# Kernel optimization log

Hardware: AMD Instinct MI355X
Metric: run time of the kernel (lower is better)

Reference implementation:

```python
import jax, jax.numpy as jnp
import numpy as np

DIM = 512
HEADS = 4
DIM_HEAD = 64          # dim // 8
INNER = HEADS * DIM_HEAD  # 256
M_LANDMARKS = 256      # dim // 2
PINV_ITERS = 6
KS = 33                # residual_conv_kernel
LN_EPS = 1e-5


def setup_inputs() -> dict:
    key = jax.random.key(0)
    ks = jax.random.split(key, 6)
    B, N = 8, 4096
    x = jax.random.normal(ks[0], (B, N, DIM), dtype=jnp.float32)
    ln_g = jnp.ones((DIM,), jnp.float32)
    ln_b = jnp.zeros((DIM,), jnp.float32)
    w_qkv = jax.random.normal(ks[1], (DIM, 3 * INNER), jnp.float32) * 0.02
    w_out = jax.random.normal(ks[2], (INNER, DIM), jnp.float32) * 0.02
    b_out = jnp.zeros((DIM,), jnp.float32)
    # depthwise Conv2d(heads, heads, (33,1), groups=heads, bias=False): OIHW = (4,1,33,1)
    w_res = jax.random.normal(ks[3], (HEADS, 1, KS, 1), jnp.float32) * 0.05
    return dict(x=x, ln_g=ln_g, ln_b=ln_b, w_qkv=w_qkv, w_out=w_out, b_out=b_out, w_res=w_res)


def moore_penrose_pinv(x, iters=PINV_ITERS):
    # x: [B, H, m, m]
    abs_x = jnp.abs(x)
    col = abs_x.sum(-1)
    row = abs_x.sum(-2)
    z = jnp.swapaxes(x, -1, -2) / (jnp.max(col) * jnp.max(row))
    I = jnp.eye(x.shape[-1], dtype=x.dtype)
    for _ in range(iters):
        xz = x @ z
        z = 0.25 * z @ (13. * I - xz @ (15. * I - xz @ (7. * I - xz)))
    return z


def reference(x, ln_g, ln_b, w_qkv, w_out, b_out, w_res):
    B, N, D = x.shape
    h, dh, m = HEADS, DIM_HEAD, M_LANDMARKS
    l = N // m  # landmark group size (N chosen divisible by m, so no padding)

    # pre-norm LayerNorm
    mu = x.mean(-1, keepdims=True)
    var = ((x - mu) ** 2).mean(-1, keepdims=True)
    xn = (x - mu) / jnp.sqrt(var + LN_EPS) * ln_g + ln_b

    qkv = xn @ w_qkv  # [B, N, 3*INNER]
    q, k, v = jnp.split(qkv, 3, axis=-1)
    to_heads = lambda t: t.reshape(B, N, h, dh).transpose(0, 2, 1, 3)  # [B,h,N,dh]
    q, k, v = to_heads(q), to_heads(k), to_heads(v)
    q = q * (dh ** -0.5)

    # landmarks: mean over contiguous groups of l  ('b h (n l) d -> b h n d')
    q_l = q.reshape(B, h, m, l, dh).mean(3)  # [B,h,m,dh]
    k_l = k.reshape(B, h, m, l, dh).mean(3)

    sim1 = jnp.einsum('bhid,bhjd->bhij', q, k_l)    # [B,h,N,m]
    sim2 = jnp.einsum('bhid,bhjd->bhij', q_l, k_l)  # [B,h,m,m]
    sim3 = jnp.einsum('bhid,bhjd->bhij', q_l, k)    # [B,h,m,N]

    a1 = jax.nn.softmax(sim1, axis=-1)
    a2 = jax.nn.softmax(sim2, axis=-1)
    a3 = jax.nn.softmax(sim3, axis=-1)

    a2_inv = moore_penrose_pinv(a2)
    out = (a1 @ a2_inv) @ (a3 @ v)  # [B,h,N,dh]

    # residual depthwise conv on v along sequence: treat as NCHW with C=h, H=N, W=dh
    conv = jax.lax.conv_general_dilated(
        v, w_res, window_strides=(1, 1),
        padding=((KS // 2, KS // 2), (0, 0)),
        feature_group_count=h,
        dimension_numbers=('NCHW', 'OIHW', 'NCHW'))
    out = out + conv

    out = out.transpose(0, 2, 1, 3).reshape(B, N, h * dh)
    out = out @ w_out + b_out  # to_out (dropout=0.1 inactive in eval)
    return x + out
```

## Files before the change

kernel.cpp:

```cpp
#include <hip/hip_runtime.h>
#include <hip/hip_bf16.h>
#include <string.h>

typedef __hip_bfloat16 bf16;
typedef __attribute__((ext_vector_type(8))) __bf16 bf16x8;
typedef __attribute__((ext_vector_type(4))) float f32x4;
typedef __attribute__((ext_vector_type(8))) unsigned short u16x8;

#define NN 4096
#define DD 512
#define MM 256
#define ROWS 32768

__device__ __forceinline__ float b2f(bf16 x) { return __bfloat162float(x); }
__device__ __forceinline__ float u2f(unsigned short u) {
  return __uint_as_float(((unsigned int)u) << 16);
}
__device__ __forceinline__ unsigned short f2bu(float v) {
  bf16 h = __float2bfloat16(v);
  return *reinterpret_cast<unsigned short*>(&h);
}
__device__ __forceinline__ float ldf(const void* p, size_t i, int f) {
  return f ? ((const float*)p)[i] : __bfloat162float(((const bf16*)p)[i]);
}
__device__ __forceinline__ void stf(void* p, size_t i, float v, int f) {
  if (f) ((float*)p)[i] = v;
  else ((bf16*)p)[i] = __float2bfloat16(v);
}

__global__ void detect_kernel(const void* x, int* flag) {
  __shared__ int red[256];
  int tid = threadIdx.x;
  const unsigned short* u = (const unsigned short*)x;
  int local = 0;
  for (int i = 0; i < 32; i++) {
    unsigned short e = (u[tid * 32 + i] >> 7) & 0xFF;
    if (e >= 0xC8) local++;
  }
  red[tid] = local; __syncthreads();
  #pragma unroll
  for (int s = 128; s > 0; s >>= 1) {
    if (tid < s) red[tid] += red[tid + s];
    __syncthreads();
  }
  if (tid == 0) *flag = (red[0] > 32) ? 1 : 0;
}

__device__ __forceinline__ float bred_max(float v, float* red) {
  int tid = threadIdx.x;
  red[tid] = v; __syncthreads();
  #pragma unroll
  for (int s = 128; s > 0; s >>= 1) {
    if (tid < s) red[tid] = fmaxf(red[tid], red[tid + s]);
    __syncthreads();
  }
  float r = red[0]; __syncthreads();
  return r;
}
__device__ __forceinline__ float bred_sum(float v, float* red) {
  int tid = threadIdx.x;
  red[tid] = v; __syncthreads();
  #pragma unroll
  for (int s = 128; s > 0; s >>= 1) {
    if (tid < s) red[tid] += red[tid + s];
    __syncthreads();
  }
  float r = red[0]; __syncthreads();
  return r;
}

__global__ void ln_stats_kernel(const void* __restrict__ x, float* __restrict__ stats,
                                const int* dflag) {
  int f = *dflag;
  int wave = threadIdx.x >> 6, lane = threadIdx.x & 63;
  int row = blockIdx.x * 4 + wave;
  size_t base = (size_t)row * DD + lane * 8;
  float v[8];
  if (f) {
    const float* xp = (const float*)x + base;
    float4 a = *(const float4*)xp;
    float4 b = *(const float4*)(xp + 4);
    v[0] = a.x; v[1] = a.y; v[2] = a.z; v[3] = a.w;
    v[4] = b.x; v[5] = b.y; v[6] = b.z; v[7] = b.w;
  } else {
    const bf16* xp = (const bf16*)x + base;
    u16x8 t = *(const u16x8*)xp;
    #pragma unroll
    for (int e = 0; e < 8; e++) v[e] = u2f(t[e]);
  }
  float s = 0, s2 = 0;
  #pragma unroll
  for (int e = 0; e < 8; e++) { s += v[e]; s2 += v[e] * v[e]; }
  #pragma unroll
  for (int off = 1; off < 64; off <<= 1) {
    s += __shfl_xor(s, off);
    s2 += __shfl_xor(s2, off);
  }
  if (lane == 0) {
    float mean = s * (1.0f / DD);
    float var = s2 * (1.0f / DD) - mean * mean;
    stats[row * 2] = mean;
    stats[row * 2 + 1] = rsqrtf(var + 1e-5f);
  }
}

__global__ void transpose_kernel(const void* __restrict__ in, bf16* __restrict__ out,
                                 int R, int Cc, long sIn, long sOut,
                                 const int* dflag, int ovr) {
  int f = (ovr >= 0) ? ovr : *dflag;
  size_t o = (size_t)blockIdx.x * 256 + threadIdx.x;
  size_t per = (size_t)R * Cc;
  size_t b = o / per, rem = o % per;
  size_t c = rem / R, r = rem % R;
  out[b * sOut + c * (size_t)R + r] = __float2bfloat16(ldf(in, b * sIn + r * (size_t)Cc + c, f));
}

__global__ __launch_bounds__(256) void gemm_qkv(
    const void* __restrict__ x, const float* __restrict__ stats,
    const void* __restrict__ g, const void* __restrict__ bb,
    const bf16* __restrict__ wT,
    bf16* __restrict__ q, bf16* __restrict__ k, bf16* __restrict__ v,
    const int* __restrict__ dflag) {
  __shared__ __align__(16) unsigned short As[128][40];
  __shared__ __align__(16) unsigned short Bs[128][40];
  __shared__ __align__(16) float gls[512];
  __shared__ __align__(16) float bls[512];
  int f = *dflag;
  int tid = threadIdx.x;
  {
    int c0 = tid, c1 = tid + 256;
    gls[c0] = ldf(g, c0, f);  gls[c1] = ldf(g, c1, f);
    bls[c0] = ldf(bb, c0, f); bls[c1] = ldf(bb, c1, f);
  }
  int m0 = blockIdx.x * 128, n0 = blockIdx.y * 128;
  int sr = tid >> 1, sh = (tid & 1) * 16;
  int wave = tid >> 6, lane = tid & 63;
  int wm = (wave & 1) * 64, wn = (wave >> 1) * 64;
  int l15 = lane & 15, quad = lane >> 4;
  int r = m0 + sr;
  float mu = stats[r * 2], rs = stats[r * 2 + 1];
  const float* xf = (const float*)x + (size_t)r * DD;
  const bf16*  xb = (const bf16*)x  + (size_t)r * DD;
  __syncthreads();
  f32x4 acc[4][4] = {};
  for (int k0 = 0; k0 < 512; k0 += 32) {
    {
      float xv[16];
      if (f) {
        const float* src = xf + k0 + sh;
        float4 t0 = *(const float4*)(src);
        float4 t1 = *(const float4*)(src + 4);
        float4 t2 = *(const float4*)(src + 8);
        float4 t3 = *(const float4*)(src + 12);
        xv[0] = t0.x; xv[1] = t0.y; xv[2]  = t0.z; xv[3]  = t0.w;
        xv[4] = t1.x; xv[5] = t1.y; xv[6]  = t1.z; xv[7]  = t1.w;
        xv[8] = t2.x; xv[9] = t2.y; xv[10] = t2.z; xv[11] = t2.w;
        xv[12] = t3.x; xv[13] = t3.y; xv[14] = t3.z; xv[15] = t3.w;
      } else {
        const bf16* src = xb + k0 + sh;
        u16x8 t0 = *(const u16x8*)(src);
        u16x8 t1 = *(const u16x8*)(src + 8);
        #pragma unroll
        for (int e = 0; e < 8; e++) { xv[e] = u2f(t0[e]); xv[8 + e] = u2f(t1[e]); }
      }
      float gv[16], bv[16];
      {
        const float* gp = &gls[k0 + sh];
        const float* bp = &bls[k0 + sh];
        #pragma unroll
        for (int e4 = 0; e4 < 4; e4++) {
          float4 gt = *(const float4*)(gp + e4 * 4);
          float4 bt = *(const float4*)(bp + e4 * 4);
          gv[e4 * 4 + 0] = gt.x; gv[e4 * 4 + 1] = gt.y; gv[e4 * 4 + 2] = gt.z; gv[e4 * 4 + 3] = gt.w;
          bv[e4 * 4 + 0] = bt.x; bv[e4 * 4 + 1] = bt.y; bv[e4 * 4 + 2] = bt.z; bv[e4 * 4 + 3] = bt.w;
        }
      }
      u16x8 w0, w1;
      #pragma unroll
      for (int e = 0; e < 8; e++) {
        float a0 = rs * gv[e];
        float a1 = rs * gv[e + 8];
        w0[e] = f2bu(xv[e] * a0 + (bv[e] - mu * a0));
        w1[e] = f2bu(xv[e + 8] * a1 + (bv[e + 8] - mu * a1));
      }
      *(u16x8*)&As[sr][sh] = w0;
      *(u16x8*)&As[sr][sh + 8] = w1;
    }
    {
      const bf16* src = wT + (size_t)(n0 + sr) * 512 + k0 + sh;
      *(u16x8*)&Bs[sr][sh] = *(const u16x8*)src;
      *(u16x8*)&Bs[sr][sh + 8] = *(const u16x8*)(src + 8);
    }
    __syncthreads();
    bf16x8 af[4], bfr[4];
    #pragma unroll
    for (int i = 0; i < 4; i++) af[i] = *(const bf16x8*)&As[wm + i * 16 + l15][quad * 8];
    #pragma unroll
    for (int j = 0; j < 4; j++) bfr[j] = *(const bf16x8*)&Bs[wn + j * 16 + l15][quad * 8];
    #pragma unroll
    for (int i = 0; i < 4; i++)
      #pragma unroll
      for (int j = 0; j < 4; j++)
        acc[i][j] = __builtin_amdgcn_mfma_f32_16x16x32_bf16(af[i], bfr[j], acc[i][j], 0, 0, 0);
    __syncthreads();
  }
  float* eps = (float*)&As[0][0];
  int half = wave & 1;
  int er = tid >> 4, ec8 = (tid & 15) * 8;
  for (int p = 0; p < 8; p++) {
    if (half == (p >> 2)) {
      int i = p & 3;
      #pragma unroll
      for (int j = 0; j < 4; j++)
        #pragma unroll
        for (int reg = 0; reg < 4; reg++)
          eps[(quad * 4 + reg) * 132 + wn + j * 16 + l15] = acc[i][j][reg];
    }
    __syncthreads();
    {
      int row = m0 + p * 16 + er;
      int c = n0 + ec8;
      int which = c >> 8, h = (c >> 6) & 3, d = c & 63;
      int b_ = row >> 12, n = row & 4095;
      const float* src = &eps[er * 132 + ec8];
      float scale = (which == 0) ? 0.125f : 1.0f;
      u16x8 o;
      #pragma unroll
      for (int e = 0; e < 8; e++) o[e] = f2bu(src[e] * scale);
      bf16* dst = (which == 0) ? q : (which == 1) ? k : v;
      *(u16x8*)(dst + ((size_t)(b_ * 4 + h) * NN + n) * 64 + d) = o;
    }
    __syncthreads();
  }
}

__global__ __launch_bounds__(256) void gemm_bt(
    const bf16* __restrict__ A, long ldA, long sA,
    const bf16* __restrict__ Bt, long ldB, long sB,
    void* __restrict__ C, long ldC, long sC,
    int N, int kLen, int nTiles, int mode,
    const void* __restrict__ bias, const void* __restrict__ resid,
    const int* __restrict__ dflag) {
  __shared__ __align__(16) unsigned short As[128][40];
  __shared__ __align__(16) unsigned short Bs[128][40];
  int tid = threadIdx.x;
  int b = blockIdx.x;
  int m0 = blockIdx.y * 128;
  int nt = blockIdx.z % nTiles, ks = blockIdx.z / nTiles;
  int n0 = nt * 128;
  long k0b = (long)ks * kLen;
  const bf16* Ab = A + (size_t)b * sA;
  const bf16* Bb = Bt + (size_t)b * sB;
  int sr = tid >> 1, sh = (tid & 1) * 16;
  int wave = tid >> 6, lane = tid & 63;
  int wm = (wave & 1) * 64, wn = (wave >> 1) * 64;
  int l15 = lane & 15, quad = lane >> 4;
  f32x4 acc[4][4] = {};
  for (int kc = 0; kc < kLen; kc += 32) {
    long k0 = k0b + kc;
    {
      const bf16* src = Ab + (size_t)(m0 + sr) * ldA + k0 + sh;
      *(u16x8*)&As[sr][sh] = *(const u16x8*)src;
      *(u16x8*)&As[sr][sh + 8] = *(const u16x8*)(src + 8);
    }
    if (n0 + sr < N) {
      const bf16* src = Bb + (size_t)(n0 + sr) * ldB + k0 + sh;
      *(u16x8*)&Bs[sr][sh] = *(const u16x8*)src;
      *(u16x8*)&Bs[sr][sh + 8] = *(const u16x8*)(src + 8);
    } else {
      u16x8 z = {};
      *(u16x8*)&Bs[sr][sh] = z;
      *(u16x8*)&Bs[sr][sh + 8] = z;
    }
    __syncthreads();
    bf16x8 af[4], bfr[4];
    #pragma unroll
    for (int i = 0; i < 4; i++) af[i] = *(const bf16x8*)&As[wm + i * 16 + l15][quad * 8];
    #pragma unroll
    for (int j = 0; j < 4; j++) bfr[j] = *(const bf16x8*)&Bs[wn + j * 16 + l15][quad * 8];
    #pragma unroll
    for (int i = 0; i < 4; i++)
      #pragma unroll
      for (int j = 0; j < 4; j++)
        acc[i][j] = __builtin_amdgcn_mfma_f32_16x16x32_bf16(af[i], bfr[j], acc[i][j], 0, 0, 0);
    __syncthreads();
  }
  if (mode == 3) {
    int f = *dflag;
    float* eps = (float*)&As[0][0];
    int half = wave & 1;
    int er = tid >> 4, ec8 = (tid & 15) * 8;
    int colb = n0 + ec8;
    float bias8[8];
    #pragma unroll
    for (int e = 0; e < 8; e++) bias8[e] = ldf(bias, colb + e, f);
    for (int p = 0; p < 8; p++) {
      if (half == (p >> 2)) {
        int i = p & 3;
        #pragma unroll
        for (int j = 0; j < 4; j++)
          #pragma unroll
          for (int reg = 0; reg < 4; reg++)
            eps[(quad * 4 + reg) * 132 + wn + j * 16 + l15] = acc[i][j][reg];
      }
      __syncthreads();
      {
        int row = m0 + p * 16 + er;
        size_t off = (size_t)row * ldC + colb;
        const float* src = &eps[er * 132 + ec8];
        if (f) {
          float* Cp = (float*)C + off;
          const float* xr = (const float*)resid + off;
          float4 r0 = *(const float4*)xr;
          float4 r1 = *(const float4*)(xr + 4);
          float4 o0, o1;
          o0.x = src[0] + bias8[0] + r0.x; o0.y = src[1] + bias8[1] + r0.y;
          o0.z = src[2] + bias8[2] + r0.z; o0.w = src[3] + bias8[3] + r0.w;
          o1.x = src[4] + bias8[4] + r1.x; o1.y = src[5] + bias8[5] + r1.y;
          o1.z = src[6] + bias8[6] + r1.z; o1.w = src[7] + bias8[7] + r1.w;
          *(float4*)Cp = o0;
          *(float4*)(Cp + 4) = o1;
        } else {
          bf16* Cp = (bf16*)C + off;
          const bf16* xr = (const bf16*)resid + off;
          u16x8 rv = *(const u16x8*)xr;
          u16x8 o;
          #pragma unroll
          for (int e = 0; e < 8; e++) o[e] = f2bu(src[e] + bias8[e] + u2f(rv[e]));
          *(u16x8*)Cp = o;
        }
      }
      __syncthreads();
    }
    return;
  }
  #pragma unroll
  for (int i = 0; i < 4; i++)
    #pragma unroll
    for (int j = 0; j < 4; j++)
      #pragma unroll
      for (int reg = 0; reg < 4; reg++) {
        int row = m0 + wm + i * 16 + quad * 4 + reg;
        int col = n0 + wn + j * 16 + l15;
        if (col < N) {
          float val = acc[i][j][reg];
          size_t off = (size_t)row * ldC + col;
          if (mode == 0) (((float*)C) + (size_t)b * sC)[off] = val;
          else if (mode == 1) (((bf16*)C) + (size_t)b * sC)[off] = __float2bfloat16(val);
          else atomicAdd(((float*)C) + (size_t)b * sC + off, val);
        }
      }
}

__global__ void landmark_kernel(const bf16* __restrict__ src, float* __restrict__ dstf,
                                bf16* __restrict__ dstb) {
  int idx = blockIdx.x * 256 + threadIdx.x;
  int d = idx & 63, j = (idx >> 6) & 255, bh = idx >> 14;
  const bf16* s = src + ((size_t)bh * NN + j * 16) * 64 + d;
  float a = 0;
  #pragma unroll
  for (int i = 0; i < 16; i++) a += b2f(s[i * 64]);
  a *= (1.0f / 16);
  dstf[idx] = a;
  dstb[idx] = __float2bfloat16(a);
}

__global__ void a2_kernel(const float* __restrict__ ql, const float* __restrict__ kl,
                          float* __restrict__ a2) {
  __shared__ float qs[64];
  __shared__ float red[256];
  int bh = blockIdx.x >> 8, i = blockIdx.x & 255, tid = threadIdx.x;
  if (tid < 64) qs[tid] = ql[((size_t)bh * MM + i) * 64 + tid];
  __syncthreads();
  const float* kr = kl + ((size_t)bh * MM + tid) * 64;
  float s = 0;
  #pragma unroll
  for (int d = 0; d < 64; d++) s += qs[d] * kr[d];
  float mx = bred_max(s, red);
  float e = __expf(s - mx);
  float sm = bred_sum(e, red);
  a2[((size_t)bh * MM + i) * MM + tid] = e / sm;
}

__global__ void colsum_max_kernel(const float* __restrict__ a2, float* __restrict__ gmax) {
  __shared__ float red[256];
  int bh = blockIdx.x, tid = threadIdx.x;
  const float* base = a2 + (size_t)bh * MM * MM + tid;
  float s0 = 0, s1 = 0, s2 = 0, s3 = 0, s4 = 0, s5 = 0, s6 = 0, s7 = 0;
  for (int i = 0; i < 256; i += 8) {
    s0 += base[(size_t)(i + 0) * MM];
    s1 += base[(size_t)(i + 1) * MM];
    s2 += base[(size_t)(i + 2) * MM];
    s3 += base[(size_t)(i + 3) * MM];
    s4 += base[(size_t)(i + 4) * MM];
    s5 += base[(size_t)(i + 5) * MM];
    s6 += base[(size_t)(i + 6) * MM];
    s7 += base[(size_t)(i + 7) * MM];
  }
  float tot = ((s0 + s1) + (s2 + s3)) + ((s4 + s5) + (s6 + s7));
  float mx = bred_max(tot, red);
  if (tid == 0) atomicMax((int*)gmax + 1, __float_as_int(mx));
}

__global__ void zinit_kernel(const float* __restrict__ a2, const float* __restrict__ gmax,
                             float* __restrict__ z) {
  int idx = blockIdx.x * 256 + threadIdx.x;
  int j = idx & 255, i = (idx >> 8) & 255, bh = idx >> 16;
  float scale = 1.0f / gmax[1];
  z[idx] = a2[((size_t)bh * MM + j) * MM + i] * scale;
}

__global__ __launch_bounds__(256) void bmm64_mfma(
    const float* __restrict__ A, const float* __restrict__ B_,
    float* __restrict__ C,
    int Nn, int Kk, long sA, long sB, long sC,
    float alpha, float beta, float gbA, float gbB) {
  __shared__ __align__(16) unsigned short Ah[64][40];
  __shared__ __align__(16) unsigned short Al[64][40];
  __shared__ __align__(16) unsigned short Bh[64][40];
  __shared__ __align__(16) unsigned short Bl[64][40];
  int bh = blockIdx.x;
  int row0 = blockIdx.y * 64, col0 = blockIdx.z * 64;
  const float* Ab = A + (size_t)bh * sA;
  const float* Bb = B_ + (size_t)bh * sB;
  int tid = threadIdx.x;
  int wave = tid >> 6, lane = tid & 63, l15 = lane & 15, quad = lane >> 4;
  int wm = (wave & 1) * 32, wn = (wave >> 1) * 32;
  int ar2 = tid >> 2, kq = (tid & 3) * 8;
  int kr = tid >> 3, n8 = (tid & 7) * 8;
  f32x4 acc[2][2] = {};
  for (int k0 = 0; k0 < Kk; k0 += 32) {
    {
      const float* src = Ab + (size_t)(row0 + ar2) * Kk + k0 + kq;
      u16x8 hi, lo;
      #pragma unroll
      for (int e = 0; e < 8; e++) {
        float a = src[e];
        unsigned short h = f2bu(a);
        hi[e] = h;
        lo[e] = f2bu(a - u2f(h));
      }
      *(u16x8*)&Ah[ar2][kq] = hi;
      *(u16x8*)&Al[ar2][kq] = lo;
    }
    {
      const float* src = Bb + (size_t)(k0 + kr) * Nn + col0 + n8;
      int kk = k0 + kr;
      #pragma unroll
      for (int e = 0; e < 8; e++) {
        float b = gbB * src[e];
        if (kk == col0 + n8 + e) b += gbA;
        unsigned short h = f2bu(b);
        Bh[n8 + e][kr] = h;
        Bl[n8 + e][kr] = f2bu(b - u2f(h));
      }
    }
    __syncthreads();
    bf16x8 ah[2], al[2], bhf[2], blf[2];
    #pragma unroll
    for (int i = 0; i < 2; i++) {
      ah[i]  = *(const bf16x8*)&Ah[wm + i * 16 + l15][quad * 8];
      al[i]  = *(const bf16x8*)&Al[wm + i * 16 + l15][quad * 8];
      bhf[i] = *(const bf16x8*)&Bh[wn + i * 16 + l15][quad * 8];
      blf[i] = *(const bf16x8*)&Bl[wn + i * 16 + l15][quad * 8];
    }
    #pragma unroll
    for (int i = 0; i < 2; i++)
      #pragma unroll
      for (int j = 0; j < 2; j++) {
        acc[i][j] = __builtin_amdgcn_mfma_f32_16x16x32_bf16(ah[i], bhf[j], acc[i][j], 0, 0, 0);
        acc[i][j] = __builtin_amdgcn_mfma_f32_16x16x32_bf16(ah[i], blf[j], acc[i][j], 0, 0, 0);
        acc[i][j] = __builtin_amdgcn_mfma_f32_16x16x32_bf16(al[i], bhf[j], acc[i][j], 0, 0, 0);
      }
    __syncthreads();
  }
  #pragma unroll
  for (int i = 0; i < 2; i++)
    #pragma unroll
    for (int j = 0; j < 2; j++)
      #pragma unroll
      for (int reg = 0; reg < 4; reg++) {
        int r = row0 + wm + i * 16 + quad * 4 + reg;
        int cc = col0 + wn + j * 16 + l15;
        C[(size_t)bh * sC + (size_t)r * Nn + cc] = alpha * (r == cc) + beta * acc[i][j][reg];
      }
}

__global__ void wmsplit_kernel(const float* __restrict__ Wm, bf16* __restrict__ h,
                               bf16* __restrict__ l) {
  int o = blockIdx.x * 256 + threadIdx.x;
  int c = o & 255, d = (o >> 8) & 63, bh = o >> 14;
  float w = Wm[(((size_t)bh << 8) + c) * 64 + d];
  unsigned short hh = f2bu(w);
  h[o] = __float2bfloat16(w);
  l[o] = __float2bfloat16(w - u2f(hh));
}

__global__ __launch_bounds__(512) void sim3_flash_kernel(
    const bf16* __restrict__ qlbf, const bf16* __restrict__ k,
    const bf16* __restrict__ vT, float* __restrict__ a3v) {
  __shared__ __align__(16) unsigned short Qs[32][72];
  __shared__ __align__(16) unsigned short Pl[8][32][72];
  __shared__ __align__(16) float OW[32][64];
  __shared__ float mW[8][32];
  __shared__ float lW[8][32];
  int tid = threadIdx.x;
  int lt = blockIdx.x;
  int bh = blockIdx.y;
  int lm0 = lt * 32;
  if (tid < 256) {
    int r = tid >> 3, s = (tid & 7) * 8;
    *(u16x8*)&Qs[r][s] = *(const u16x8*)(qlbf + ((size_t)bh * 256 + lm0 + r) * 64 + s);
  }
  {
    float4 z = {};
    ((float4*)OW)[tid] = z;
  }
  __syncthreads();
  int wid = tid >> 6, lane = tid & 63, l15 = lane & 15, quad = lane >> 4;
  const bf16* kb = k + (size_t)bh * (NN * 64);
  const bf16* vb = vT + (size_t)bh * 262144;
  unsigned short* Pw = &Pl[wid][0][0];
  float m_[2] = {-1e30f, -1e30f};
  float l_[2] = {0.f, 0.f};
  f32x4 acc_o[2][4] = {};
  for (int ch = 0; ch < 8; ch++) {
    int kvb = wid * 512 + ch * 64;
    f32x4 acc_s[4][2] = {};
    #pragma unroll
    for (int kc = 0; kc < 2; kc++) {
      bf16x8 kf[4], qf[2];
      #pragma unroll
      for (int i = 0; i < 4; i++)
        kf[i] = *(const bf16x8*)(kb + (size_t)(kvb + i * 16 + l15) * 64 + kc * 32 + quad * 8);
      #pragma unroll
      for (int j = 0; j < 2; j++)
        qf[j] = *(const bf16x8*)&Qs[j * 16 + l15][kc * 32 + quad * 8];
      #pragma unroll
      for (int i = 0; i < 4; i++)
        #pragma unroll
        for (int j = 0; j < 2; j++)
          acc_s[i][j] = __builtin_amdgcn_mfma_f32_16x16x32_bf16(kf[i], qf[j], acc_s[i][j], 0, 0, 0);
    }
    float scl[2];
    #pragma unroll
    for (int js = 0; js < 2; js++) {
      float cm = acc_s[0][js][0];
      #pragma unroll
      for (int i = 0; i < 4; i++)
        #pragma unroll
        for (int reg = 0; reg < 4; reg++) cm = fmaxf(cm, acc_s[i][js][reg]);
      cm = fmaxf(cm, __shfl_xor(cm, 16));
      cm = fmaxf(cm, __shfl_xor(cm, 32));
      float mn = fmaxf(m_[js], cm);
      scl[js] = __expf(m_[js] - mn);
      m_[js] = mn;
    }
    #pragma unroll
    for (int io = 0; io < 2; io++)
      #pragma unroll
      for (int reg = 0; reg < 4; reg++) {
        float sb = __shfl(scl[io], quad * 4 + reg);
        #pragma unroll
        for (int jd = 0; jd < 4; jd++) acc_o[io][jd][reg] *= sb;
      }
    #pragma unroll
    for (int js = 0; js < 2; js++) {
      float cs = 0;
      #pragma unroll
      for (int i = 0; i < 4; i++)
        #pragma unroll
        for (int reg = 0; reg < 4; reg++) {
          float p = __expf(acc_s[i][js][reg] - m_[js]);
          cs += p;
          Pw[(js * 16 + l15) * 72 + i * 16 + quad * 4 + reg] = f2bu(p);
        }
      cs += __shfl_xor(cs, 16);
      cs += __shfl_xor(cs, 32);
      l_[js] = l_[js] * scl[js] + cs;
    }
    #pragma unroll
    for (int kc2 = 0; kc2 < 2; kc2++) {
      bf16x8 pf[2], vf[4];
      #pragma unroll
      for (int io = 0; io < 2; io++)
        pf[io] = *(const bf16x8*)&Pw[(io * 16 + l15) * 72 + kc2 * 32 + quad * 8];
      #pragma unroll
      for (int jd = 0; jd < 4; jd++)
        vf[jd] = *(const bf16x8*)(vb + (size_t)(jd * 16 + l15) * 4096 + kvb + kc2 * 32 + quad * 8);
      #pragma unroll
      for (int io = 0; io < 2; io++)
        #pragma unroll
        for (int jd = 0; jd < 4; jd++)
          acc_o[io][jd] = __builtin_amdgcn_mfma_f32_16x16x32_bf16(pf[io], vf[jd], acc_o[io][jd], 0, 0, 0);
    }
  }
  if (quad == 0) {
    mW[wid][l15] = m_[0]; mW[wid][16 + l15] = m_[1];
    lW[wid][l15] = l_[0]; lW[wid][16 + l15] = l_[1];
  }
  __syncthreads();
  #pragma unroll
  for (int io = 0; io < 2; io++)
    #pragma unroll
    for (int reg = 0; reg < 4; reg++) {
      int lm = io * 16 + quad * 4 + reg;
      float ms = mW[0][lm];
      #pragma unroll
      for (int w = 1; w < 8; w++) ms = fmaxf(ms, mW[w][lm]);
      float ls = 0;
      #pragma unroll
      for (int w = 0; w < 8; w++) ls += __expf(mW[w][lm] - ms) * lW[w][lm];
      float fac = __expf(mW[wid][lm] - ms) / ls;
      #pragma unroll
      for (int jd = 0; jd < 4; jd++)
        atomicAdd(&OW[lm][jd * 16 + l15], acc_o[io][jd][reg] * fac);
    }
  __syncthreads();
  {
    float4 o = ((float4*)OW)[tid];
    *(float4*)(a3v + (size_t)bh * 16384 + (size_t)lm0 * 64 + tid * 4) = o;
  }
}

__global__ __launch_bounds__(256) void attn1_pv_kernel(
    const bf16* __restrict__ q, const bf16* __restrict__ klbf,
    const bf16* __restrict__ wmt_h, const bf16* __restrict__ wmt_l,
    float* __restrict__ p1f, int bh0) {
  __shared__ __align__(16) unsigned short Qs[32][72];
  __shared__ __align__(16) unsigned short Ks[256][72];
  __shared__ __align__(16) unsigned short Wh[64][40];
  __shared__ __align__(16) unsigned short Wl[64][40];
  __shared__ float redm[4][32];
  __shared__ float reds[4][32];
  int tid = threadIdx.x;
  int bhl = blockIdx.y, bh = bh0 + bhl;
  int n0 = blockIdx.x * 32;
  const bf16* qb = q + ((size_t)bh * NN + n0) * 64;
  const bf16* kb = klbf + (size_t)bh * 16384;
  {
    int r = tid >> 3, s = (tid & 7) * 8;
    *(u16x8*)&Qs[r][s] = *(const u16x8*)(qb + (size_t)r * 64 + s);
  }
  {
    const bf16* src = kb + (size_t)tid * 64;
    #pragma unroll
    for (int s8 = 0; s8 < 8; s8++) *(u16x8*)&Ks[tid][s8 * 8] = *(const u16x8*)(src + s8 * 8);
  }
  __syncthreads();
  int wave = tid >> 6, lane = tid & 63, l15 = lane & 15, quad = lane >> 4;
  f32x4 acc[2][4] = {};
  #pragma unroll
  for (int kc = 0; kc < 64; kc += 32) {
    bf16x8 af[2], bfr[4];
    #pragma unroll
    for (int i = 0; i < 2; i++) af[i] = *(const bf16x8*)&Qs[i * 16 + l15][kc + quad * 8];
    #pragma unroll
    for (int j = 0; j < 4; j++) bfr[j] = *(const bf16x8*)&Ks[wave * 64 + j * 16 + l15][kc + quad * 8];
    #pragma unroll
    for (int i = 0; i < 2; i++)
      #pragma unroll
      for (int j = 0; j < 4; j++)
        acc[i][j] = __builtin_amdgcn_mfma_f32_16x16x32_bf16(af[i], bfr[j], acc[i][j], 0, 0, 0);
  }
  float lm[2][4], ls[2][4], rinv[2][4];
  #pragma unroll
  for (int i = 0; i < 2; i++)
    #pragma unroll
    for (int reg = 0; reg < 4; reg++)
      lm[i][reg] = fmaxf(fmaxf(acc[i][0][reg], acc[i][1][reg]),
                         fmaxf(acc[i][2][reg], acc[i][3][reg]));
  #pragma unroll
  for (int off = 1; off < 16; off <<= 1)
    #pragma unroll
    for (int i = 0; i < 2; i++)
      #pragma unroll
      for (int reg = 0; reg < 4; reg++) lm[i][reg] = fmaxf(lm[i][reg], __shfl_xor(lm[i][reg], off));
  if (l15 == 0)
    #pragma unroll
    for (int i = 0; i < 2; i++)
      #pragma unroll
      for (int reg = 0; reg < 4; reg++) redm[wave][i * 16 + quad * 4 + reg] = lm[i][reg];
  __syncthreads();
  #pragma unroll
  for (int i = 0; i < 2; i++)
    #pragma unroll
    for (int reg = 0; reg < 4; reg++) {
      int r = i * 16 + quad * 4 + reg;
      rinv[i][reg] = fmaxf(fmaxf(redm[0][r], redm[1][r]), fmaxf(redm[2][r], redm[3][r]));
      ls[i][reg] = 0;
    }
  #pragma unroll
  for (int i = 0; i < 2; i++)
    #pragma unroll
    for (int j = 0; j < 4; j++)
      #pragma unroll
      for (int reg = 0; reg < 4; reg++) {
        float e = __expf(acc[i][j][reg] - rinv[i][reg]);
        acc[i][j][reg] = e;
        ls[i][reg] += e;
      }
  #pragma unroll
  for (int off = 1; off < 16; off <<= 1)
    #pragma unroll
    for (int i = 0; i < 2; i++)
      #pragma unroll
      for (int reg = 0; reg < 4; reg++) ls[i][reg] += __shfl_xor(ls[i][reg], off);
  if (l15 == 0)
    #pragma unroll
    for (int i = 0; i < 2; i++)
      #pragma unroll
      for (int reg = 0; reg < 4; reg++) reds[wave][i * 16 + quad * 4 + reg] = ls[i][reg];
  __syncthreads();
  #pragma unroll
  for (int i = 0; i < 2; i++)
    #pragma unroll
    for (int reg = 0; reg < 4; reg++) {
      int r = i * 16 + quad * 4 + reg;
      rinv[i][reg] = 1.0f / (reds[0][r] + reds[1][r] + reds[2][r] + reds[3][r]);
    }
  unsigned short* Pb = &Ks[0][0];
  #pragma unroll
  for (int i = 0; i < 2; i++)
    #pragma unroll
    for (int j = 0; j < 4; j++)
      #pragma unroll
      for (int reg = 0; reg < 4; reg++) {
        float pv = acc[i][j][reg] * rinv[i][reg];
        unsigned short h = f2bu(pv);
        int row = i * 16 + quad * 4 + reg;
        int col = wave * 64 + j * 16 + l15;
        Pb[row * 264 + col] = h;
        Pb[8448 + row * 264 + col] = f2bu(pv - u2f(h));
      }
  const bf16* whp = wmt_h + (size_t)bh * 16384;
  const bf16* wlp = wmt_l + (size_t)bh * 16384;
  int wd = tid >> 2, wc = (tid & 3) * 8;
  int iw = wave & 1, dw = (wave >> 1) * 32;
  f32x4 accp[2] = {};
  for (int kc = 0; kc < 256; kc += 32) {
    __syncthreads();
    *(u16x8*)&Wh[wd][wc] = *(const u16x8*)(whp + (size_t)wd * 256 + kc + wc);
    *(u16x8*)&Wl[wd][wc] = *(const u16x8*)(wlp + (size_t)wd * 256 + kc + wc);
    __syncthreads();
    bf16x8 ah = *(const bf16x8*)&Pb[(iw * 16 + l15) * 264 + kc + quad * 8];
    bf16x8 al = *(const bf16x8*)&Pb[8448 + (iw * 16 + l15) * 264 + kc + quad * 8];
    #pragma unroll
    for (int jj = 0; jj < 2; jj++) {
      bf16x8 bh2 = *(const bf16x8*)&Wh[dw + jj * 16 + l15][quad * 8];
      bf16x8 bl2 = *(const bf16x8*)&Wl[dw + jj * 16 + l15][quad * 8];
      accp[jj] = __builtin_amdgcn_mfma_f32_16x16x32_bf16(ah, bh2, accp[jj], 0, 0, 0);
      accp[jj] = __builtin_amdgcn_mfma_f32_16x16x32_bf16(ah, bl2, accp[jj], 0, 0, 0);
      accp[jj] = __builtin_amdgcn_mfma_f32_16x16x32_bf16(al, bh2, accp[jj], 0, 0, 0);
    }
  }
  #pragma unroll
  for (int jj = 0; jj < 2; jj++)
    #pragma unroll
    for (int reg = 0; reg < 4; reg++) {
      int r = iw * 16 + quad * 4 + reg;
      int d = dw + jj * 16 + l15;
      int n = n0 + r;
      p1f[((size_t)bhl * NN + n) * 64 + d] = accp[jj][reg];
    }
}

__global__ __launch_bounds__(256) void conv_add_kernel(
    const float* __restrict__ p1, const bf16* __restrict__ v,
    const void* __restrict__ wres, bf16* __restrict__ y, const int* __restrict__ dflag,
    int bh0) {
  __shared__ __align__(16) unsigned short Vs[96][64];
  int f = *dflag;
  int tid = threadIdx.x;
  int bhl = blockIdx.y, bh = bh0 + bhl;
  int n0 = blockIdx.x * 64;
  int h = bh & 3, b_ = bh >> 2;
  const bf16* vb = v + (size_t)bh * (NN * 64);
  for (int rr = tid; rr < 384; rr += 256) {
    int r = rr >> 2, s = (rr & 3) * 16;
    int n = n0 - 16 + r;
    if (n >= 0 && n < NN) {
      *(u16x8*)&Vs[r][s] = *(const u16x8*)(vb + (size_t)n * 64 + s);
      *(u16x8*)&Vs[r][s + 8] = *(const u16x8*)(vb + (size_t)n * 64 + s + 8);
    } else {
      u16x8 z = {};
      *(u16x8*)&Vs[r][s] = z; *(u16x8*)&Vs[r][s + 8] = z;
    }
  }
  float w33[33];
  #pragma unroll
  for (int kk = 0; kk < 33; kk++) w33[kk] = ldf(wres, h * 33 + kk, f);
  __syncthreads();
  int d = tid & 63, rb = tid >> 6;
  for (int ii = 0; ii < 16; ii++) {
    int nl = ii * 4 + rb;
    float cv = 0;
    #pragma unroll
    for (int kk = 0; kk < 33; kk++) cv += w33[kk] * u2f(Vs[nl + kk][d]);
    int n = n0 + nl;
    float pv = p1[((size_t)bhl * NN + n) * 64 + d];
    y[((size_t)b_ * NN + n) * 256 + h * 64 + d] = __float2bfloat16(pv + cv);
  }
}

extern "C" void kernel_launch(void* const* d_in, const int* in_sizes, int n_in,
                              void* d_out, int out_size, void* d_ws, size_t ws_size,
                              hipStream_t stream) {
  const void* x     = d_in[0];
  const void* ln_g  = d_in[1];
  const void* ln_b  = d_in[2];
  const void* w_qkv = d_in[3];
  const void* w_out = d_in[4];
  const void* b_out = d_in[5];
  const void* w_res = d_in[6];

  float* ws    = (float*)d_ws;
  float* gmax  = ws;
  int*   dflag = (int*)(ws + 2);
  float* stats = ws + 256;
  bf16*  woutT = (bf16*)(stats + 65536);
  float* qlf   = (float*)(stats + 65536 + 65536);
  float* klf   = qlf + 524288;
  bf16*  qlbf  = (bf16*)(klf + 524288);
  bf16*  klbf  = qlbf + 524288;
  float* a3v   = (float*)(klbf + 524288);
  float* Wm    = a3v + 524288;
  float* a2    = Wm + 524288;
  bf16*  q     = (bf16*)(a2 + 2097152);
  bf16*  k     = q + 8388608;
  bf16*  v     = k + 8388608;
  bf16*  y     = k;
  bf16*  wmt_h = (bf16*)a2;
  bf16*  wmt_l = wmt_h + 524288;

  char* dob = (char*)d_out;
  bf16* wqkvT = (bf16*)dob;
  bf16* vTfull = (bf16*)dob;
  float* W0   = (float*)dob;
  float* W1   = (float*)(dob + (8u << 20));
  float* W2   = (float*)(dob + (16u << 20));
  float* W3   = (float*)(dob + (24u << 20));
  float* p1f  = (float*)dob;

  detect_kernel<<<1, 256, 0, stream>>>(x, dflag);
  hipMemsetAsync(gmax, 0, 2 * sizeof(float), stream);
  ln_stats_kernel<<<8192, 256, 0, stream>>>(x, stats, dflag);

  transpose_kernel<<<1536, 256, 0, stream>>>(w_qkv, wqkvT, 512, 768, 0, 0, dflag, -1);
  transpose_kernel<<<512, 256, 0, stream>>>(w_out, woutT, 256, 512, 0, 0, dflag, -1);

  gemm_qkv<<<dim3(256, 6), 256, 0, stream>>>(x, stats, ln_g, ln_b, wqkvT, q, k, v, dflag);

  landmark_kernel<<<2048, 256, 0, stream>>>(q, qlf, qlbf);
  landmark_kernel<<<2048, 256, 0, stream>>>(k, klf, klbf);

  transpose_kernel<<<32768, 256, 0, stream>>>(v, vTfull, 4096, 64, 262144, 262144, dflag, 0);
  sim3_flash_kernel<<<dim3(8, 32), 512, 0, stream>>>(qlbf, k, vTfull, a3v);

  a2_kernel<<<8192, 256, 0, stream>>>(qlf, klf, a2);
  colsum_max_kernel<<<32, 256, 0, stream>>>(a2, gmax);
  zinit_kernel<<<8192, 256, 0, stream>>>(a2, gmax, W0);

  float* zi = W0; float* f1 = W1; float* f2 = W2; float* f3 = W3;
  for (int it = 0; it < 6; it++) {
    bmm64_mfma<<<dim3(32, 4, 4), 256, 0, stream>>>(a2, zi, f1, 256, 256, 65536, 65536, 65536, 0.f, 1.f, 0.f, 1.f);
    bmm64_mfma<<<dim3(32, 4, 4), 256, 0, stream>>>(f1, f1, f2, 256, 256, 65536, 65536, 65536, 15.f, -1.f, 7.f, -1.f);
    bmm64_mfma<<<dim3(32, 4, 4), 256, 0, stream>>>(f1, f2, f3, 256, 256, 65536, 65536, 65536, 13.f, -1.f, 0.f, 1.f);
    bmm64_mfma<<<dim3(32, 4, 4), 256, 0, stream>>>(zi, f3, f2, 256, 256, 65536, 65536, 65536, 0.f, 0.25f, 0.f, 1.f);
    float* nzi = f2; f2 = f1; f1 = zi; zi = nzi;
  }

  bmm64_mfma<<<dim3(32, 4, 1), 256, 0, stream>>>(zi, a3v, Wm, 64, 256, 65536, 16384, 16384, 0.f, 1.f, 0.f, 1.f);

  wmsplit_kernel<<<2048, 256, 0, stream>>>(Wm, wmt_h, wmt_l);

  attn1_pv_kernel<<<dim3(128, 32), 256, 0, stream>>>(q, klbf, wmt_h, wmt_l, p1f, 0);
  conv_add_kernel<<<dim3(64, 32), 256, 0, stream>>>(p1f, v, w_res, y, dflag, 0);

  gemm_bt<<<dim3(1, 256, 4), 256, 0, stream>>>(
      y, 256, 0, woutT, 256, 0,
      d_out, 512, 0, 512, 256, 4, 3, b_out, x, dflag);
}
```

Measured before the change: 850.1 us.

## Fuse residual depthwise conv into attn1 PV kernel and drop LDS staging of Wm

Merges the separate conv_add kernel into the attn1 PV kernel, so the fp32 intermediate p1f (32x4096x64 floats) is never written to and re-read from global memory, and one launch is removed. The Wm hi/lo operands are now loaded straight from global memory (cached) instead of being staged through shared memory with two barriers per k-chunk. P hi/lo bf16 stores are packed into 32-bit LDS writes using lane shuffles. The conv reuses the Ks shared buffer for a 64-row V halo tile. This adds conv work and V loads to each block, and the direct global B-operand loads may have more latency.

```diff
diff --git a/kernel.cpp b/kernel.cpp
--- a/kernel.cpp
+++ b/kernel.cpp
@@ -623,19 +623,21 @@
   }
 }
 
-__global__ __launch_bounds__(256) void attn1_pv_kernel(
+__global__ __launch_bounds__(256) void attn1_pv_conv_kernel(
     const bf16* __restrict__ q, const bf16* __restrict__ klbf,
     const bf16* __restrict__ wmt_h, const bf16* __restrict__ wmt_l,
-    float* __restrict__ p1f, int bh0) {
+    const bf16* __restrict__ v, const void* __restrict__ wres,
+    bf16* __restrict__ y, const int* __restrict__ dflag) {
   __shared__ __align__(16) unsigned short Qs[32][72];
   __shared__ __align__(16) unsigned short Ks[256][72];
-  __shared__ __align__(16) unsigned short Wh[64][40];
-  __shared__ __align__(16) unsigned short Wl[64][40];
   __shared__ float redm[4][32];
   __shared__ float reds[4][32];
+  __shared__ float wls[33];
   int tid = threadIdx.x;
-  int bhl = blockIdx.y, bh = bh0 + bhl;
+  int bh = blockIdx.y;
   int n0 = blockIdx.x * 32;
+  int h = bh & 3, b_ = bh >> 2;
+  if (tid < 33) wls[tid] = ldf(wres, h * 33 + tid, *dflag);
   const bf16* qb = q + ((size_t)bh * NN + n0) * 64;
   const bf16* kb = klbf + (size_t)bh * 16384;
   {
@@ -719,7 +721,7 @@
       int r = i * 16 + quad * 4 + reg;
       rinv[i][reg] = 1.0f / (reds[0][r] + reds[1][r] + reds[2][r] + reds[3][r]);
     }
-  unsigned short* Pb = &Ks[0][0];
+  unsigned int* P32 = (unsigned int*)&Ks[0][0];
   #pragma unroll
   for (int i = 0; i < 2; i++)
     #pragma unroll
@@ -727,31 +729,60 @@
       #pragma unroll
       for (int reg = 0; reg < 4; reg++) {
         float pv = acc[i][j][reg] * rinv[i][reg];
-        unsigned short h = f2bu(pv);
+        unsigned int hh = f2bu(pv);
+        unsigned int ll = f2bu(pv - u2f((unsigned short)hh));
+        unsigned int ph = (unsigned int)__shfl_xor((int)hh, 1);
+        unsigned int pl = (unsigned int)__shfl_xor((int)ll, 1);
         int row = i * 16 + quad * 4 + reg;
         int col = wave * 64 + j * 16 + l15;
-        Pb[row * 264 + col] = h;
-        Pb[8448 + row * 264 + col] = f2bu(pv - u2f(h));
-      }
+        int dwi = row * 132 + (col >> 1);
+        if ((l15 & 1) == 0) P32[dwi] = hh | (ph << 16);
+        else P32[4224 + dwi] = pl | (ll << 16);
+      }
+  __syncthreads();
+  const unsigned short* Pb = &Ks[0][0];
   const bf16* whp = wmt_h + (size_t)bh * 16384;
   const bf16* wlp = wmt_l + (size_t)bh * 16384;
-  int wd = tid >> 2, wc = (tid & 3) * 8;
   int iw = wave & 1, dw = (wave >> 1) * 32;
   f32x4 accp[2] = {};
+  #pragma unroll
   for (int kc = 0; kc < 256; kc += 32) {
-    __syncthreads();
-    *(u16x8*)&Wh[wd][wc] = *(const u16x8*)(whp + (size_t)wd * 256 + kc + wc);
-    *(u16x8*)&Wl[wd][wc] = *(const u16x8*)(wlp + (size_t)wd * 256 + kc + wc);
-    __syncthreads();
     bf16x8 ah = *(const bf16x8*)&Pb[(iw * 16 + l15) * 264 + kc + quad * 8];
     bf16x8 al = *(const bf16x8*)&Pb[8448 + (iw * 16 + l15) * 264 + kc + quad * 8];
     #pragma unroll
     for (int jj = 0; jj < 2; jj++) {
-      bf16x8 bh2 = *(const bf16x8*)&Wh[dw + jj * 16 + l15][quad * 8];
-      bf16x8 bl2 = *(const bf16x8*)&Wl[dw + jj * 16 + l15][quad * 8];
+      size_t woff = (size_t)(dw + jj * 16 + l15) * 256 + kc + quad * 8;
+      bf16x8 bh2 = *(const bf16x8*)(whp + woff);
+      bf16x8 bl2 = *(const bf16x8*)(wlp + woff);
       accp[jj] = __builtin_amdgcn_mfma_f32_16x16x32_bf16(ah, bh2, accp[jj], 0, 0, 0);
       accp[jj] = __builtin_amdgcn_mfma_f32_16x16x32_bf16(ah, bl2, accp[jj], 0, 0, 0);
       accp[jj] = __builtin_amdgcn_mfma_f32_16x16x32_bf16(al, bh2, accp[jj], 0, 0, 0);
+    }
+  }
+  __syncthreads();
+  unsigned short* Vs = &Ks[0][0];
+  const bf16* vb = v + (size_t)bh * (NN * 64);
+  #pragma unroll
+  for (int cc = 0; cc < 2; cc++) {
+    int c = cc * 256 + tid;
+    int r = c >> 3, s8 = (c & 7) * 8;
+    int n = n0 - 16 + r;
+    u16x8 t = {};
+    if (n >= 0 && n < NN) t = *(const u16x8*)(vb + (size_t)n * 64 + s8);
+    *(u16x8*)&Vs[r * 72 + s8] = t;
+  }
+  __syncthreads();
+  float cv[2][4] = {};
+  for (int kk = 0; kk < 33; kk++) {
+    float wv = wls[kk];
+    #pragma unroll
+    for (int jj = 0; jj < 2; jj++) {
+      int d = dw + jj * 16 + l15;
+      #pragma unroll
+      for (int reg = 0; reg < 4; reg++) {
+        int r = iw * 16 + quad * 4 + reg;
+        cv[jj][reg] += wv * u2f(Vs[(r + kk) * 72 + d]);
+      }
     }
   }
   #pragma unroll
@@ -761,46 +792,8 @@
       int r = iw * 16 + quad * 4 + reg;
       int d = dw + jj * 16 + l15;
       int n = n0 + r;
-      p1f[((size_t)bhl * NN + n) * 64 + d] = accp[jj][reg];
-    }
-}
-
-__global__ __launch_bounds__(256) void conv_add_kernel(
-    const float* __restrict__ p1, const bf16* __restrict__ v,
-    const void* __restrict__ wres, bf16* __restrict__ y, const int* __restrict__ dflag,
-    int bh0) {
-  __shared__ __align__(16) unsigned short Vs[96][64];
-  int f = *dflag;
-  int tid = threadIdx.x;
-  int bhl = blockIdx.y, bh = bh0 + bhl;
-  int n0 = blockIdx.x * 64;
-  int h = bh & 3, b_ = bh >> 2;
-  const bf16* vb = v + (size_t)bh * (NN * 64);
-  for (int rr = tid; rr < 384; rr += 256) {
-    int r = rr >> 2, s = (rr & 3) * 16;
-    int n = n0 - 16 + r;
-    if (n >= 0 && n < NN) {
-      *(u16x8*)&Vs[r][s] = *(const u16x8*)(vb + (size_t)n * 64 + s);
-      *(u16x8*)&Vs[r][s + 8] = *(const u16x8*)(vb + (size_t)n * 64 + s + 8);
-    } else {
-      u16x8 z = {};
-      *(u16x8*)&Vs[r][s] = z; *(u16x8*)&Vs[r][s + 8] = z;
-    }
-  }
-  float w33[33];
-  #pragma unroll
-  for (int kk = 0; kk < 33; kk++) w33[kk] = ldf(wres, h * 33 + kk, f);
-  __syncthreads();
-  int d = tid & 63, rb = tid >> 6;
-  for (int ii = 0; ii < 16; ii++) {
-    int nl = ii * 4 + rb;
-    float cv = 0;
-    #pragma unroll
-    for (int kk = 0; kk < 33; kk++) cv += w33[kk] * u2f(Vs[nl + kk][d]);
-    int n = n0 + nl;
-    float pv = p1[((size_t)bhl * NN + n) * 64 + d];
-    y[((size_t)b_ * NN + n) * 256 + h * 64 + d] = __float2bfloat16(pv + cv);
-  }
+      y[((size_t)b_ * NN + n) * 256 + h * 64 + d] = __float2bfloat16(accp[jj][reg] + cv[jj][reg]);
+    }
 }
 
 extern "C" void kernel_launch(void* const* d_in, const int* in_sizes, int n_in,
@@ -840,7 +833,6 @@
   float* W1   = (float*)(dob + (8u << 20));
   float* W2   = (float*)(dob + (16u << 20));
   float* W3   = (float*)(dob + (24u << 20));
-  float* p1f  = (float*)dob;
 
   detect_kernel<<<1, 256, 0, stream>>>(x, dflag);
   hipMemsetAsync(gmax, 0, 2 * sizeof(float), stream);
@@ -874,8 +866,7 @@
 
   wmsplit_kernel<<<2048, 256, 0, stream>>>(Wm, wmt_h, wmt_l);
 
-  attn1_pv_kernel<<<dim3(128, 32), 256, 0, stream>>>(q, klbf, wmt_h, wmt_l, p1f, 0);
-  conv_add_kernel<<<dim3(64, 32), 256, 0, stream>>>(p1f, v, w_res, y, dflag, 0);
+  attn1_pv_conv_kernel<<<dim3(128, 32), 256, 0, stream>>>(q, klbf, wmt_h, wmt_l, v, w_res, y, dflag);
 
   gemm_bt<<<dim3(1, 256, 4), 256, 0, stream>>>(
       y, 256, 0, woutT, 256, 0,
```

Result: no change. 863.9 us (+1.6%).
